# Performance work log

Measured on AMD Instinct MI355X. Metric: run time of the kernel, lower is better.

Reference implementation:

```python
import jax, jax.numpy as jnp
import numpy as np

EPS = 1e-5


def _bn(x, g, b):
    # BatchNorm1d in training mode: batch mean, biased variance, eps=1e-5
    m = jnp.mean(x, axis=0)
    v = jnp.var(x, axis=0)
    return (x - m) * jax.lax.rsqrt(v + EPS) * g + b


def setup_inputs() -> dict:
    key = jax.random.key(0)
    ks = jax.random.split(key, 16)
    B, N, F, H = 4096, 128, 4, 32
    w = lambda k, o, i: jax.random.normal(k, (o, i), jnp.float32) * 0.3
    d = {
        'u': jax.random.normal(ks[0], (B, N, F), jnp.float32),
        'mask': jnp.ones((B * N, 1), jnp.int32),
        # MLPphi params
        'p_bn1_g': jnp.ones((F,), jnp.float32), 'p_bn1_b': jnp.zeros((F,), jnp.float32), 'p_w1': w(ks[1], H, F),
        'p_bn2_g': jnp.ones((H,), jnp.float32), 'p_bn2_b': jnp.zeros((H,), jnp.float32), 'p_w2': w(ks[2], H, H),
        'p_bn3_g': jnp.ones((H,), jnp.float32), 'p_bn3_b': jnp.zeros((H,), jnp.float32), 'p_w3': w(ks[3], H, H),
        # MLPomega params
        'o_bn1_g': jnp.ones((F,), jnp.float32), 'o_bn1_b': jnp.zeros((F,), jnp.float32), 'o_w1': w(ks[4], H, F),
        'o_bn2_g': jnp.ones((H,), jnp.float32), 'o_bn2_b': jnp.zeros((H,), jnp.float32), 'o_w2': w(ks[5], H, H),
        'o_bn3_g': jnp.ones((H,), jnp.float32), 'o_bn3_b': jnp.zeros((H,), jnp.float32), 'o_w3': w(ks[6], H, H),
        # MLPtheta params
        't_bn1_g': jnp.ones((H,), jnp.float32), 't_bn1_b': jnp.zeros((H,), jnp.float32), 't_w1': w(ks[7], H, H),
        't_bn2_g': jnp.ones((H,), jnp.float32), 't_bn2_b': jnp.zeros((H,), jnp.float32), 't_w2': w(ks[8], H, H),
        't_bn3_g': jnp.ones((H,), jnp.float32), 't_bn3_b': jnp.zeros((H,), jnp.float32), 't_w3': w(ks[9], H, H),
        't_bn4_g': jnp.ones((H,), jnp.float32), 't_bn4_b': jnp.zeros((H,), jnp.float32),
        't_w4': w(ks[10], 1, H), 't_b4': jnp.zeros((1,), jnp.float32),
    }
    return d


def _forward(u, mask,
             p_bn1_g, p_bn1_b, p_w1, p_bn2_g, p_bn2_b, p_w2, p_bn3_g, p_bn3_b, p_w3,
             o_bn1_g, o_bn1_b, o_w1, o_bn2_g, o_bn2_b, o_w2, o_bn3_g, o_bn3_b, o_w3,
             t_bn1_g, t_bn1_b, t_w1, t_bn2_g, t_bn2_b, t_w2, t_bn3_g, t_bn3_b, t_w3,
             t_bn4_g, t_bn4_b, t_w4, t_b4):
    B, N, F = u.shape
    H = p_w1.shape[0]
    u_flat = u.reshape(-1, F)  # (B*N, F)

    # MLPphi: three BN+Linear(no bias)+Tanh blocks with residual adds (dropout=identity in eval)
    o1 = jnp.tanh(_bn(u_flat, p_bn1_g, p_bn1_b) @ p_w1.T)
    o2 = jnp.tanh(_bn(o1, p_bn2_g, p_bn2_b) @ p_w2.T)
    o3 = jnp.tanh(_bn(o1 + o2, p_bn3_g, p_bn3_b) @ p_w3.T)
    x_main = (o1 + o2 + o3).reshape(B, N, H)

    # MLPomega: BN+Linear+Tanh x2, BN+Linear, softmax over hidden dim (dim=1 of flat), then masked_fill
    a = jnp.tanh(_bn(u_flat, o_bn1_g, o_bn1_b) @ o_w1.T)
    a = jnp.tanh(_bn(a, o_bn2_g, o_bn2_b) @ o_w2.T)
    a = _bn(a, o_bn3_g, o_bn3_b) @ o_w3.T
    a = jax.nn.softmax(a, axis=1)
    a = jnp.where(mask == 0, -jnp.inf, a)
    x_attn = a.reshape(B, N, H)

    # attention pooling over neighbors
    x = jnp.sum(x_main * x_attn, axis=1)  # (B, H)

    x = jnp.tanh(_bn(x, t_bn1_g, t_bn1_b) @ t_w1.T)
    x = jnp.tanh(_bn(x, t_bn2_g, t_bn2_b) @ t_w2.T)
    x = jnp.tanh(_bn(x, t_bn3_g, t_bn3_b) @ t_w3.T)
    x = _bn(x, t_bn4_g, t_bn4_b) @ t_w4.T + t_b4
    return x


def reference(u, mask,
              p_bn1_g, p_bn1_b, p_w1, p_bn2_g, p_bn2_b, p_w2, p_bn3_g, p_bn3_b, p_w3,
              o_bn1_g, o_bn1_b, o_w1, o_bn2_g, o_bn2_b, o_w2, o_bn3_g, o_bn3_b, o_w3,
              t_bn1_g, t_bn1_b, t_w1, t_bn2_g, t_bn2_b, t_w2, t_bn3_g, t_bn3_b, t_w3,
              t_bn4_g, t_bn4_b, t_w4, t_b4):
    return _forward(u, mask,
                    p_bn1_g, p_bn1_b, p_w1, p_bn2_g, p_bn2_b, p_w2, p_bn3_g, p_bn3_b, p_w3,
                    o_bn1_g, o_bn1_b, o_w1, o_bn2_g, o_bn2_b, o_w2, o_bn3_g, o_bn3_b, o_w3,
                    t_bn1_g, t_bn1_b, t_w1, t_bn2_g, t_bn2_b, t_w2, t_bn3_g, t_bn3_b, t_w3,
                    t_bn4_g, t_bn4_b, t_w4, t_b4)
```

## Files before the change

### kernel.cpp

```cpp
#include <hip/hip_runtime.h>

typedef unsigned int u32;
typedef unsigned short u16;
typedef __attribute__((ext_vector_type(8))) _Float16 half8;
typedef __attribute__((ext_vector_type(4))) float f32x4;

#define ROWS  524288
#define BROWS 4096
#define EPS   1e-5f

#define S_U   0
#define S_O1  8
#define S_A1  72
#define S_O12 136
#define S_A2  200
#define S_X   264
#define S_X1  328
#define S_X2  392
#define S_X3  456
#define SHARD 1024
#define NSH   64

#define XSTR 40

__device__ __forceinline__ float bl(u32 u){ return __uint_as_float(u << 16); }
__device__ __forceinline__ float bh(u32 u){ return __uint_as_float(u & 0xFFFF0000u); }
__device__ __forceinline__ float b2f(u16 h){ return __uint_as_float(((u32)h) << 16); }
__device__ __forceinline__ u16 f2b(float f){
  u32 u = __float_as_uint(f);
  return (u16)((u + 0x7FFFu + ((u >> 16) & 1u)) >> 16);
}
__device__ __forceinline__ u16 f2h(float f){ _Float16 h = (_Float16)f; return __builtin_bit_cast(u16, h); }
__device__ __forceinline__ float h2f(u16 x){ return (float)__builtin_bit_cast(_Float16, x); }
__device__ __forceinline__ u32 pack2h(float a, float b){
  auto v = __builtin_amdgcn_cvt_pkrtz(a, b);
  return __builtin_bit_cast(u32, v);
}
__device__ __forceinline__ float lo16(u32 w){ return h2f((u16)(w & 0xFFFF)); }
__device__ __forceinline__ float hi16(u32 w){ return h2f((u16)(w >> 16)); }
__device__ __forceinline__ void unpk4(uint2 v, float* d){
  d[0]=lo16(v.x); d[1]=hi16(v.x); d[2]=lo16(v.y); d[3]=hi16(v.y);
}

__device__ __forceinline__ float tanh_fast(float x){
  float e = __expf(2.0f * x);
  return 1.0f - 2.0f * __builtin_amdgcn_rcpf(e + 1.0f);
}

template<bool F32>
__device__ __forceinline__ float rdp(const void* p, int i){
  if (F32) return ((const float*)p)[i];
  return b2f(((const u16*)p)[i]);
}
template<bool F32>
__device__ __forceinline__ void load_u4(const void* u, int r, float* f){
  if (F32){
    float4 v = ((const float4*)u)[r];
    f[0]=v.x; f[1]=v.y; f[2]=v.z; f[3]=v.w;
  } else {
    uint2 v = ((const uint2*)u)[r];
    f[0]=bl(v.x); f[1]=bh(v.x); f[2]=bl(v.y); f[3]=bh(v.y);
  }
}

__device__ __forceinline__ void g2lrow(const u16* __restrict__ g, int r, u16* X, int tid){
  const uint4* src = (const uint4*)&g[(size_t)r*32];
  uint4* dst = (uint4*)&X[tid*XSTR];
#pragma unroll
  for (int c=0;c<4;++c) dst[c] = src[c];
}
__device__ __forceinline__ void l2grow(const u16* X, int tid, u16* __restrict__ g, int r){
  const uint4* src = (const uint4*)&X[tid*XSTR];
  uint4* dst = (uint4*)&g[(size_t)r*32];
#pragma unroll
  for (int c=0;c<4;++c) dst[c] = src[c];
}

__global__ void k_detect(const u16* __restrict__ u, int* __restrict__ flag){
  int t = threadIdx.x;
  int bad = 0;
  for (int i = t*4; i < t*4+4; ++i){
    int e = (u[i] >> 7) & 0xFF;
    bad += (e >= 0x90) ? 1 : 0;
  }
#pragma unroll
  for (int off = 32; off >= 1; off >>= 1) bad += __shfl_down(bad, off);
  if (t == 0) *flag = (bad >= 4) ? 1 : 0;
}

template<bool F32>
__device__ __forceinline__ void stats_u_body(const void* __restrict__ u, float* __restrict__ S){
  int tid = blockIdx.x*blockDim.x + threadIdx.x;
  int nt  = gridDim.x*blockDim.x;
  float s[4]={0,0,0,0}, q[4]={0,0,0,0};
  for (int r = tid; r < ROWS; r += nt){
    float f[4]; load_u4<F32>(u, r, f);
#pragma unroll
    for (int k=0;k<4;++k){ s[k]+=f[k]; q[k]+=f[k]*f[k]; }
  }
#pragma unroll
  for (int off=32; off>=1; off>>=1){
#pragma unroll
    for (int k=0;k<4;++k){ s[k]+=__shfl_down(s[k],off); q[k]+=__shfl_down(q[k],off); }
  }
  if ((threadIdx.x & 63) == 0){
    float* Sh = S + (blockIdx.x & (NSH-1))*SHARD;
#pragma unroll
    for (int k=0;k<4;++k){ atomicAdd(&Sh[S_U+k], s[k]); atomicAdd(&Sh[S_U+4+k], q[k]); }
  }
}
__global__ __launch_bounds__(256) void k_stats_u(const void* __restrict__ u, float* __restrict__ S,
                                                 const int* __restrict__ flag){
  if (*flag) stats_u_body<true>(u,S); else stats_u_body<false>(u,S);
}

__device__ __forceinline__ void prep_u(const float* __restrict__ S, float* mr, int tid){
  if (tid < 4){
    float s=0.f, q=0.f;
    for (int sh=0; sh<NSH; ++sh){
      s += S[sh*SHARD + S_U + tid];
      q += S[sh*SHARD + S_U + 4 + tid];
    }
    float m = s*(1.0f/ROWS);
    float var = q*(1.0f/ROWS) - m*m;
    mr[tid]   = m;
    mr[4+tid] = rsqrtf(var + EPS);
  }
  __syncthreads();
}
template<bool F32>
__device__ __forceinline__ void bn_u_l(const float* mr, const void* g, const void* b,
                                       const float* f, float* xn){
#pragma unroll
  for (int k=0;k<4;++k)
    xn[k] = (f[k]-mr[k])*(rdp<F32>(g,k)*mr[4+k]) + rdp<F32>(b,k);
}

template<bool F32>
__device__ __forceinline__ void chain1_to_lds(const float* xn, const void* W1, u16* Xrow){
  u32 buf[16];
#pragma unroll
  for (int jp=0; jp<16; ++jp){
    int j0 = 2*jp, j1 = 2*jp+1;
    float a0 = tanh_fast(xn[0]*rdp<F32>(W1,j0*4+0) + xn[1]*rdp<F32>(W1,j0*4+1)
                       + xn[2]*rdp<F32>(W1,j0*4+2) + xn[3]*rdp<F32>(W1,j0*4+3));
    float a1 = tanh_fast(xn[0]*rdp<F32>(W1,j1*4+0) + xn[1]*rdp<F32>(W1,j1*4+1)
                       + xn[2]*rdp<F32>(W1,j1*4+2) + xn[3]*rdp<F32>(W1,j1*4+3));
    buf[jp] = pack2h(a0, a1);
  }
#pragma unroll
  for (int c=0;c<4;++c){
    uint4 v; v.x = buf[c*4]; v.y = buf[c*4+1]; v.z = buf[c*4+2]; v.w = buf[c*4+3];
    *(uint4*)&Xrow[c*8] = v;
  }
}

template<bool F32>
__device__ __forceinline__ void fold2(const float* __restrict__ S, int offA, int offB,
    const void* gA, const void* bA, const void* WA,
    const void* gB, const void* bB, const void* WB,
    u16* Wt, float* Cb, float* scr )
{
  int tid = threadIdx.x;
  if (tid < 64){
    int L = tid>>5, k = tid&31;
    const void* g = L? gB:gA; const void* b = L? bB:bA;
    int off = L? offB:offA;
    float s=0.f, q=0.f;
    for (int sh=0; sh<NSH; ++sh){
      s += S[sh*SHARD + off + k];
      q += S[sh*SHARD + off + 32 + k];
    }
    float m    = s*(1.0f/ROWS);
    float var  = q*(1.0f/ROWS) - m*m;
    float rstd = rsqrtf(var+EPS);
    float sc = rdp<F32>(g,k)*rstd;
    scr[tid]    = sc;
    scr[64+tid] = rdp<F32>(b,k) - m*sc;
  }
  __syncthreads();
  if (tid < 64){
    int L = tid>>5, j = tid&31;
    const void* W = L? WB:WA;
    float c = 0.f;
#pragma unroll
    for (int k=0;k<32;++k){
      float Wv = rdp<F32>(W, j*32+k);
      Wt[(L*32+j)*XSTR + k] = f2h(Wv * scr[(L<<5)|k]);
      c += Wv * scr[64 + ((L<<5)|k)];
    }
    Cb[L*32+j] = c;
  }
  __syncthreads();
}

template<bool F32>
__device__ __forceinline__ void fold4(const float* __restrict__ S,
    int off0,int off1,int off2,int off3,
    const void* g0,const void* b0,const void* W0,
    const void* g1,const void* b1,const void* W1,
    const void* g2,const void* b2,const void* W2,
    const void* g3,const void* b3,const void* W3,
    u16* Wt, float* Cb, float* scr )
{
  int tid = threadIdx.x;
  __shared__ float scr2[256];
  if (tid < 128){
    int L = tid>>5, k = tid&31;
    const void* g = (L==0)?g0:(L==1)?g1:(L==2)?g2:g3;
    const void* b = (L==0)?b0:(L==1)?b1:(L==2)?b2:b3;
    int off = (L==0)?off0:(L==1)?off1:(L==2)?off2:off3;
    float s=0.f, q=0.f;
    for (int sh=0; sh<NSH; ++sh){
      s += S[sh*SHARD + off + k];
      q += S[sh*SHARD + off + 32 + k];
    }
    float m    = s*(1.0f/ROWS);
    float var  = q*(1.0f/ROWS) - m*m;
    float rstd = rsqrtf(var+EPS);
    float sc = rdp<F32>(g,k)*rstd;
    scr[tid]  = sc;
    scr2[tid] = rdp<F32>(b,k) - m*sc;
  }
  __syncthreads();
  if (tid < 128){
    int L = tid>>5, j = tid&31;
    const void* W = (L==0)?W0:(L==1)?W1:(L==2)?W2:W3;
    float c = 0.f;
#pragma unroll
    for (int k=0;k<32;++k){
      float Wv = rdp<F32>(W, j*32+k);
      Wt[(L*32+j)*XSTR + k] = f2h(Wv * scr[(L<<5)|k]);
      c += Wv * scr2[(L<<5)|k];
    }
    Cb[L*32+j] = c;
  }
  __syncthreads();
}

#define KIND_TANH          0
#define KIND_TANHRES       2
#define KIND_TANHRES_ATREG 3
template<int KIND>
__device__ __forceinline__ void mfma_layer(u16* X, const u16* Wt, const float* Cb,
                                           int L, int wv, int lane, const u32* at_pk)
{
  int ln15 = lane & 15, quad = lane >> 4;
  half8 w0 = *(const half8*)&Wt[(L*32 + ln15     )*XSTR + quad*8];
  half8 w1 = *(const half8*)&Wt[(L*32 + ln15 + 16)*XSTR + quad*8];
  float bias0[4], bias1[4];
#pragma unroll
  for (int reg=0;reg<4;++reg){
    bias0[reg] = Cb[L*32 +      quad*4 + reg];
    bias1[reg] = Cb[L*32 + 16 + quad*4 + reg];
  }
  int rowbase = wv*64;
#pragma unroll
  for (int Mt=0; Mt<4; ++Mt){
    int s = rowbase + Mt*16 + ln15;
    half8 bfr = *(const half8*)&X[s*XSTR + quad*8];
    f32x4 c0 = {0.f,0.f,0.f,0.f}, c1 = {0.f,0.f,0.f,0.f};
    c0 = __builtin_amdgcn_mfma_f32_16x16x32_f16(w0, bfr, c0, 0,0,0);
    c1 = __builtin_amdgcn_mfma_f32_16x16x32_f16(w1, bfr, c1, 0,0,0);
    float o0[4], o1v[4];
    if (KIND == KIND_TANHRES || KIND == KIND_TANHRES_ATREG){
      unpk4(*(const uint2*)&X[s*XSTR +      quad*4], o0);
      unpk4(*(const uint2*)&X[s*XSTR + 16 + quad*4], o1v);
    }
    float a0v[4], a1v[4];
    if (KIND == KIND_TANHRES_ATREG){
      a0v[0]=lo16(at_pk[Mt*4+0]); a0v[1]=hi16(at_pk[Mt*4+0]);
      a0v[2]=lo16(at_pk[Mt*4+1]); a0v[3]=hi16(at_pk[Mt*4+1]);
      a1v[0]=lo16(at_pk[Mt*4+2]); a1v[1]=hi16(at_pk[Mt*4+2]);
      a1v[2]=lo16(at_pk[Mt*4+3]); a1v[3]=hi16(at_pk[Mt*4+3]);
    }
    float v0[4], v1[4];
#pragma unroll
    for (int reg=0;reg<4;++reg){
      float a = c0[reg] + bias0[reg];
      float b = c1[reg] + bias1[reg];
      if (KIND == KIND_TANH){ a = tanh_fast(a); b = tanh_fast(b); }
      else if (KIND == KIND_TANHRES){ a = o0[reg] + tanh_fast(a); b = o1v[reg] + tanh_fast(b); }
      else if (KIND == KIND_TANHRES_ATREG){
        a = (o0[reg] + tanh_fast(a)) * a0v[reg];
        b = (o1v[reg] + tanh_fast(b)) * a1v[reg];
      }
      v0[reg] = a; v1[reg] = b;
    }
    uint2 w0o, w1o;
    w0o.x = pack2h(v0[0], v0[1]); w0o.y = pack2h(v0[2], v0[3]);
    w1o.x = pack2h(v1[0], v1[1]); w1o.y = pack2h(v1[2], v1[3]);
    *(uint2*)&X[s*XSTR +      quad*4] = w0o;
    *(uint2*)&X[s*XSTR + 16 + quad*4] = w1o;
  }
}

__device__ __forceinline__ void mfma_logits_softmax(const u16* X, const u16* Wt, const float* Cb,
    int L, int wv, int lane, const int* __restrict__ mask, int maskbase, u32* at_pk)
{
  int ln15 = lane & 15, quad = lane >> 4;
  half8 w0 = *(const half8*)&Wt[(L*32 + ln15     )*XSTR + quad*8];
  half8 w1 = *(const half8*)&Wt[(L*32 + ln15 + 16)*XSTR + quad*8];
  float bias0[4], bias1[4];
#pragma unroll
  for (int reg=0;reg<4;++reg){
    bias0[reg] = Cb[L*32 +      quad*4 + reg];
    bias1[reg] = Cb[L*32 + 16 + quad*4 + reg];
  }
  int rowbase = wv*64;
#pragma unroll
  for (int Mt=0; Mt<4; ++Mt){
    int s = rowbase + Mt*16 + ln15;
    half8 bfr = *(const half8*)&X[s*XSTR + quad*8];
    f32x4 c0 = {0.f,0.f,0.f,0.f}, c1 = {0.f,0.f,0.f,0.f};
    c0 = __builtin_amdgcn_mfma_f32_16x16x32_f16(w0, bfr, c0, 0,0,0);
    c1 = __builtin_amdgcn_mfma_f32_16x16x32_f16(w1, bfr, c1, 0,0,0);
    float l0[4], l1[4];
#pragma unroll
    for (int reg=0;reg<4;++reg){ l0[reg] = c0[reg]+bias0[reg]; l1[reg] = c1[reg]+bias1[reg]; }
    float mx = l0[0];
#pragma unroll
    for (int reg=1;reg<4;++reg) mx = fmaxf(mx, l0[reg]);
#pragma unroll
    for (int reg=0;reg<4;++reg) mx = fmaxf(mx, l1[reg]);
    mx = fmaxf(mx, __shfl_xor(mx, 16));
    mx = fmaxf(mx, __shfl_xor(mx, 32));
    float sum = 0.f;
#pragma unroll
    for (int reg=0;reg<4;++reg){ l0[reg] = __expf(l0[reg]-mx); sum += l0[reg]; }
#pragma unroll
    for (int reg=0;reg<4;++reg){ l1[reg] = __expf(l1[reg]-mx); sum += l1[reg]; }
    sum += __shfl_xor(sum, 16);
    sum += __shfl_xor(sum, 32);
    float inv = __builtin_amdgcn_rcpf(sum);
    bool mz = (mask[maskbase + Mt*16 + ln15] == 0);
#pragma unroll
    for (int reg=0;reg<4;++reg){
      l0[reg] *= inv; l1[reg] *= inv;
      if (mz){ l0[reg] = -__builtin_inff(); l1[reg] = -__builtin_inff(); }
    }
    at_pk[Mt*4+0] = pack2h(l0[0], l0[1]);
    at_pk[Mt*4+1] = pack2h(l0[2], l0[3]);
    at_pk[Mt*4+2] = pack2h(l1[0], l1[1]);
    at_pk[Mt*4+3] = pack2h(l1[2], l1[3]);
  }
}

__device__ __forceinline__ void reduce_f16(const u16* X, float* lds2,
                                           float* __restrict__ S, int offS, int shard)
{
  int tid = threadIdx.x;
  __syncthreads();
  {
    int j = tid & 31, seg = tid >> 5;
    float s=0.f, q=0.f;
    for (int q2=0;q2<32;++q2){
      float v = h2f(X[(seg*32+q2)*XSTR + j]);
      s += v; q = fmaf(v,v,q);
    }
    lds2[seg*32+j] = s;
    lds2[256 + seg*32+j] = q;
  }
  __syncthreads();
  if (tid < 64){
    int j = tid & 31; bool isq = tid >= 32;
    const float* src = lds2 + (isq?256:0);
    float tot=0.f;
#pragma unroll
    for (int sg=0;sg<8;++sg) tot += src[sg*32+j];
    atomicAdd(&S[shard*SHARD + offS + (isq?32:0) + j], tot);
  }
  __syncthreads();
}

__device__ __forceinline__ void reduce_f32(const float* Xs, float* lds2,
                                           float* __restrict__ S, int offS, int shard)
{
  int tid = threadIdx.x;
  __syncthreads();
  {
    int j = tid & 31, seg = tid >> 5;
    float s=0.f, q=0.f;
    for (int q2=0;q2<32;++q2){
      float v = Xs[(seg*32+q2)*33 + j];
      s += v; q = fmaf(v,v,q);
    }
    lds2[seg*32+j] = s;
    lds2[256 + seg*32+j] = q;
  }
  __syncthreads();
  if (tid < 64){
    int j = tid & 31; bool isq = tid >= 32;
    const float* src = lds2 + (isq?256:0);
    float tot=0.f;
#pragma unroll
    for (int sg=0;sg<8;++sg) tot += src[sg*32+j];
    atomicAdd(&S[shard*SHARD + offS + (isq?32:0) + j], tot);
  }
  __syncthreads();
}

template<bool F32, bool MAT>
__device__ __forceinline__ void pass1_body(const void* __restrict__ u,
    const void* pg1, const void* pb1, const void* pw1,
    const void* og1, const void* ob1, const void* ow1,
    float* __restrict__ S, u16* __restrict__ o1g, u16* __restrict__ a1g,
    float* Xs, float* lds2, float* mr)
{
  int tid = threadIdx.x;
  int r = blockIdx.x*256 + tid;
  int shard = blockIdx.x & (NSH-1);
  prep_u(S, mr, tid);
  float f[4]; load_u4<F32>(u,r,f);
  float xn[4];
  float* Xp = Xs + tid*33;

  bn_u_l<F32>(mr, pg1, pb1, f, xn);
  {
    u32 buf[16];
#pragma unroll
    for (int jp=0;jp<16;++jp){
      int j0=2*jp, j1=2*jp+1;
      float a0 = tanh_fast(xn[0]*rdp<F32>(pw1,j0*4+0) + xn[1]*rdp<F32>(pw1,j0*4+1)
                         + xn[2]*rdp<F32>(pw1,j0*4+2) + xn[3]*rdp<F32>(pw1,j0*4+3));
      float a1 = tanh_fast(xn[0]*rdp<F32>(pw1,j1*4+0) + xn[1]*rdp<F32>(pw1,j1*4+1)
                         + xn[2]*rdp<F32>(pw1,j1*4+2) + xn[3]*rdp<F32>(pw1,j1*4+3));
      Xp[j0]=a0; Xp[j1]=a1;
      if (MAT) buf[jp] = pack2h(a0,a1);
    }
    if (MAT){
      uint4* dst = (uint4*)&o1g[(size_t)r*32];
#pragma unroll
      for (int c=0;c<4;++c){ uint4 v; v.x=buf[c*4]; v.y=buf[c*4+1]; v.z=buf[c*4+2]; v.w=buf[c*4+3]; dst[c]=v; }
    }
  }
  reduce_f32(Xs, lds2, S, S_O1, shard);

  bn_u_l<F32>(mr, og1, ob1, f, xn);
  {
    u32 buf[16];
#pragma unroll
    for (int jp=0;jp<16;++jp){
      int j0=2*jp, j1=2*jp+1;
      float a0 = tanh_fast(xn[0]*rdp<F32>(ow1,j0*4+0) + xn[1]*rdp<F32>(ow1,j0*4+1)
                         + xn[2]*rdp<F32>(ow1,j0*4+2) + xn[3]*rdp<F32>(ow1,j0*4+3));
      float a1 = tanh_fast(xn[0]*rdp<F32>(ow1,j1*4+0) + xn[1]*rdp<F32>(ow1,j1*4+1)
                         + xn[2]*rdp<F32>(ow1,j1*4+2) + xn[3]*rdp<F32>(ow1,j1*4+3));
      Xp[j0]=a0; Xp[j1]=a1;
      if (MAT) buf[jp] = pack2h(a0,a1);
    }
    if (MAT){
      uint4* dst = (uint4*)&a1g[(size_t)r*32];
#pragma unroll
      for (int c=0;c<4;++c){ uint4 v; v.x=buf[c*4]; v.y=buf[c*4+1]; v.z=buf[c*4+2]; v.w=buf[c*4+3]; dst[c]=v; }
    }
  }
  reduce_f32(Xs, lds2, S, S_A1, shard);
}
template<bool MAT>
__global__ __launch_bounds__(256) void k_pass1(const void* __restrict__ u,
    const void* pg1, const void* pb1, const void* pw1,
    const void* og1, const void* ob1, const void* ow1,
    float* __restrict__ S, u16* o1g, u16* a1g, const int* __restrict__ flag){
  __shared__ float Xs[256*33];
  __shared__ float lds2[512];
  __shared__ float mr[8];
  if (*flag) pass1_body<true ,MAT>(u,pg1,pb1,pw1,og1,ob1,ow1,S,o1g,a1g,Xs,lds2,mr);
  else       pass1_body<false,MAT>(u,pg1,pb1,pw1,og1,ob1,ow1,S,o1g,a1g,Xs,lds2,mr);
}

template<bool F32, bool MAT>
__device__ __forceinline__ void pass2_body(const void* __restrict__ u,
    const void* pg1, const void* pb1, const void* pw1,
    const void* og1, const void* ob1, const void* ow1,
    const void* pg2, const void* pb2, const void* pw2,
    const void* og2, const void* ob2, const void* ow2,
    float* __restrict__ S,
    const u16* __restrict__ o1g, const u16* __restrict__ a1g,
    u16* __restrict__ o12g, u16* __restrict__ a2g,
    u16* X, u16* Wt, float* Cb, float* lds2, float* mr)
{
  int tid = threadIdx.x;
  int wv = tid >> 6, lane = tid & 63;
  int r = blockIdx.x*256 + tid;
  int shard = blockIdx.x & (NSH-1);
  if (!MAT) prep_u(S, mr, tid);
  fold2<F32>(S, S_O1, S_A1, pg2,pb2,pw2, og2,ob2,ow2, Wt, Cb, lds2);

  float f[4], xn[4];
  if (!MAT) load_u4<F32>(u,r,f);

  if (MAT) g2lrow(o1g, r, X, tid);
  else { bn_u_l<F32>(mr, pg1, pb1, f, xn); chain1_to_lds<F32>(xn, pw1, X + tid*XSTR); }
  mfma_layer<KIND_TANHRES>(X, Wt, Cb, 0, wv, lane, 0);
  reduce_f16(X, lds2, S, S_O12, shard);
  if (MAT) l2grow(X, tid, o12g, r);

  if (MAT) g2lrow(a1g, r, X, tid);
  else { bn_u_l<F32>(mr, og1, ob1, f, xn); chain1_to_lds<F32>(xn, ow1, X + tid*XSTR); }
  mfma_layer<KIND_TANH  >(X, Wt, Cb, 1, wv, lane, 0);
  reduce_f16(X, lds2, S, S_A2, shard);
  if (MAT) l2grow(X, tid, a2g, r);
}
template<bool MAT>
__global__ __launch_bounds__(256) void k_pass2(const void* __restrict__ u,
    const void* pg1, const void* pb1, const void* pw1,
    const void* og1, const void* ob1, const void* ow1,
    const void* pg2, const void* pb2, const void* pw2,
    const void* og2, const void* ob2, const void* ow2,
    float* __restrict__ S, const u16* o1g, const u16* a1g, u16* o12g, u16* a2g,
    const int* __restrict__ flag){
  __shared__ u16 X[256*XSTR];
  __shared__ u16 Wt[2*32*XSTR];
  __shared__ float Cb[64];
  __shared__ float lds2[512];
  __shared__ float mr[8];
  if (*flag) pass2_body<true ,MAT>(u,pg1,pb1,pw1,og1,ob1,ow1,pg2,pb2,pw2,og2,ob2,ow2,S,o1g,a1g,o12g,a2g,X,Wt,Cb,lds2,mr);
  else       pass2_body<false,MAT>(u,pg1,pb1,pw1,og1,ob1,ow1,pg2,pb2,pw2,og2,ob2,ow2,S,o1g,a1g,o12g,a2g,X,Wt,Cb,lds2,mr);
}

template<bool F32, bool MAT>
__device__ __forceinline__ void pass3_body(const void* __restrict__ u, const int* __restrict__ mask,
    const void* pg1, const void* pb1, const void* pw1,
    const void* og1, const void* ob1, const void* ow1,
    const void* pg2, const void* pb2, const void* pw2,
    const void* og2, const void* ob2, const void* ow2,
    const void* pg3, const void* pb3, const void* pw3,
    const void* og3, const void* ob3, const void* ow3,
    const u16* __restrict__ o12g, const u16* __restrict__ a2g,
    float* __restrict__ x, float* __restrict__ S,
    u16* X, u16* Wt, float* Cb, float* red2, float* mr)
{
  int tid = threadIdx.x;
  int wv = tid >> 6, lane = tid & 63;
  int r = blockIdx.x*256 + tid;
  if (!MAT) prep_u(S, mr, tid);
  if (MAT){
    fold2<F32>(S, S_A2, S_O12, og3,ob3,ow3, pg3,pb3,pw3, Wt, Cb, red2);
  } else {
    fold4<F32>(S, S_A1, S_A2, S_O1, S_O12,
               og2,ob2,ow2, og3,ob3,ow3, pg2,pb2,pw2, pg3,pb3,pw3,
               Wt, Cb, red2);
  }

  float f[4], xn[4];
  if (!MAT) load_u4<F32>(u,r,f);
  u32 at_pk[16];
  int maskbase = blockIdx.x*256 + wv*64;

  if (MAT) g2lrow(a2g, r, X, tid);
  else { bn_u_l<F32>(mr, og1, ob1, f, xn); chain1_to_lds<F32>(xn, ow1, X + tid*XSTR);
         mfma_layer<KIND_TANH>(X, Wt, Cb, 0, wv, lane, 0); }
  mfma_logits_softmax(X, Wt, Cb, MAT?0:1, wv, lane, mask, maskbase, at_pk);

  if (MAT) g2lrow(o12g, r, X, tid);
  else { bn_u_l<F32>(mr, pg1, pb1, f, xn); chain1_to_lds<F32>(xn, pw1, X + tid*XSTR);
         mfma_layer<KIND_TANHRES>(X, Wt, Cb, 2, wv, lane, 0); }
  mfma_layer<KIND_TANHRES_ATREG>(X, Wt, Cb, MAT?1:3, wv, lane, at_pk);

  __syncthreads();
  {
    int jj = tid & 31, cgrp = (tid >> 5) & 3, half = tid >> 7;
    float s2 = 0.f;
    for (int q2=0;q2<32;++q2) s2 += h2f(X[(half*128 + cgrp*32 + q2)*XSTR + jj]);
    red2[tid] = s2;
  }
  __syncthreads();
  if (tid < 64){
    int half = tid >> 5, j = tid & 31;
    float v = red2[half*128+j] + red2[half*128+32+j] + red2[half*128+64+j] + red2[half*128+96+j];
    x[(blockIdx.x*2 + half)*32 + j] = v;
    float* Sh = S + (blockIdx.x & (NSH-1))*SHARD;
    atomicAdd(&Sh[S_X+j], v);
    atomicAdd(&Sh[S_X+32+j], v*v);
  }
}
template<bool MAT>
__global__ __launch_bounds__(256) void k_pass3(const void* __restrict__ u, const int* __restrict__ mask,
    const void* pg1, const void* pb1, const void* pw1,
    const void* og1, const void* ob1, const void* ow1,
    const void* pg2, const void* pb2, const void* pw2,
    const void* og2, const void* ob2, const void* ow2,
    const void* pg3, const void* pb3, const void* pw3,
    const void* og3, const void* ob3, const void* ow3,
    const u16* o12g, const u16* a2g,
    float* __restrict__ x, float* __restrict__ S, const int* __restrict__ flag){
  __shared__ u16 X [256*XSTR];
  __shared__ u16 Wt[4*32*XSTR];
  __shared__ float Cb[128];
  __shared__ float red2[256];
  __shared__ float mr[8];
  if (*flag) pass3_body<true ,MAT>(u,mask,pg1,pb1,pw1,og1,ob1,ow1,pg2,pb2,pw2,og2,ob2,ow2,
                                   pg3,pb3,pw3,og3,ob3,ow3,o12g,a2g,x,S,X,Wt,Cb,red2,mr);
  else       pass3_body<false,MAT>(u,mask,pg1,pb1,pw1,og1,ob1,ow1,pg2,pb2,pw2,og2,ob2,ow2,
                                   pg3,pb3,pw3,og3,ob3,ow3,o12g,a2g,x,S,X,Wt,Cb,red2,mr);
}

template<bool F32>
__device__ __forceinline__ void theta_body(const float* __restrict__ X, float* __restrict__ S, int offin,
    const void* g, const void* bt, const void* W, float* __restrict__ Y, int offout,
    float* lds, float* lds2)
{
  int r = blockIdx.x*blockDim.x + threadIdx.x;
  int tid = threadIdx.x;
  int shard = blockIdx.x & (NSH-1);
  if (tid < 32){
    float s=0.f, q=0.f;
    for (int sh=0; sh<NSH; ++sh){
      s += S[sh*SHARD + offin + tid];
      q += S[sh*SHARD + offin + 32 + tid];
    }
    float m = s*(1.0f/BROWS);
    float var = q*(1.0f/BROWS) - m*m;
    lds2[tid]    = m;
    lds2[32+tid] = rsqrtf(var + EPS);
  }
  __syncthreads();
  float* Xp = lds + tid*33;
#pragma unroll
  for (int k=0;k<32;++k){
    Xp[k] = (X[(size_t)r*32+k] - lds2[k]) * (rdp<F32>(g,k)*lds2[32+k]) + rdp<F32>(bt,k);
  }
  float out[32];
#pragma unroll
  for (int j=0;j<32;++j){
    float acc = 0.f;
#pragma unroll
    for (int k=0;k<32;++k) acc = fmaf(rdp<F32>(W, j*32+k), Xp[k], acc);
    out[j] = tanh_fast(acc);
    Y[(size_t)r*32+j] = out[j];
  }
  __syncthreads();
#pragma unroll
  for (int j=0;j<32;++j) Xp[j] = out[j];
  reduce_f32(lds, lds2, S, offout, shard);
}
__global__ __launch_bounds__(256) void k_theta(const float* X, float* S, int offin,
    const void* g, const void* bt, const void* W, float* Y, int offout, const int* __restrict__ flag){
  __shared__ float lds[256*33];
  __shared__ float lds2[512];
  if (*flag) theta_body<true >(X,S,offin,g,bt,W,Y,offout,lds,lds2);
  else       theta_body<false>(X,S,offin,g,bt,W,Y,offout,lds,lds2);
}

template<bool F32>
__device__ __forceinline__ void theta4_body(const float* __restrict__ X, const float* __restrict__ S, int offin,
    const void* g, const void* bt, const void* w4, const void* b4, void* out, float* ms)
{
  int r = blockIdx.x*blockDim.x + threadIdx.x;
  int tid = threadIdx.x;
  if (tid < 32){
    float s=0.f, q=0.f;
    for (int sh=0; sh<NSH; ++sh){
      s += S[sh*SHARD + offin + tid];
      q += S[sh*SHARD + offin + 32 + tid];
    }
    float m = s*(1.0f/BROWS);
    float var = q*(1.0f/BROWS) - m*m;
    ms[tid]    = m;
    ms[32+tid] = rsqrtf(var + EPS);
  }
  __syncthreads();
  float acc = rdp<F32>(b4, 0);
#pragma unroll
  for (int k=0;k<32;++k){
    float xnv = (X[(size_t)r*32+k] - ms[k]) * (rdp<F32>(g,k)*ms[32+k]) + rdp<F32>(bt,k);
    acc = fmaf(rdp<F32>(w4,k), xnv, acc);
  }
  if (F32) ((float*)out)[r] = acc;
  else     ((u16*)out)[r]  = f2b(acc);
}
__global__ __launch_bounds__(256) void k_theta4(const float* X, const float* S, int offin,
    const void* g, const void* bt, const void* w4, const void* b4, void* out, const int* __restrict__ flag){
  __shared__ float ms[64];
  if (*flag) theta4_body<true >(X,S,offin,g,bt,w4,b4,out,ms);
  else       theta4_body<false>(X,S,offin,g,bt,w4,b4,out,ms);
}

extern "C" void kernel_launch(void* const* d_in, const int* in_sizes, int n_in,
                              void* d_out, int out_size, void* d_ws, size_t ws_size,
                              hipStream_t stream)
{
  const void* u    = d_in[0];
  const int*  mask = (const int*)d_in[1];
  const void *pg1=d_in[2],  *pb1=d_in[3],  *pw1=d_in[4];
  const void *pg2=d_in[5],  *pb2=d_in[6],  *pw2=d_in[7];
  const void *pg3=d_in[8],  *pb3=d_in[9],  *pw3=d_in[10];
  const void *og1=d_in[11], *ob1=d_in[12], *ow1=d_in[13];
  const void *og2=d_in[14], *ob2=d_in[15], *ow2=d_in[16];
  const void *og3=d_in[17], *ob3=d_in[18], *ow3=d_in[19];
  const void *tg1=d_in[20], *tb1=d_in[21], *tw1=d_in[22];
  const void *tg2=d_in[23], *tb2=d_in[24], *tw2=d_in[25];
  const void *tg3=d_in[26], *tb3=d_in[27], *tw3=d_in[28];
  const void *tg4=d_in[29], *tb4=d_in[30], *tw4=d_in[31], *tbb4=d_in[32];

  char* ws = (char*)d_ws;
  int*   flag = (int*)ws;
  float* S    = (float*)(ws + 4096);
  float* x    = (float*)(ws + 524288);
  float* x1 = x  + BROWS*32;
  float* x2 = x1 + BROWS*32;
  float* x3 = x2 + BROWS*32;

  const size_t MB = 1024*1024;
  u16* o1g  = (u16*)(ws + 8*MB);
  u16* a1g  = (u16*)(ws + 40*MB);
  u16* o12g = (u16*)(ws + 72*MB);
  u16* a2g  = (u16*)(ws + 104*MB);
  bool MAT = ws_size >= 137*MB;

  (void)hipMemsetAsync(ws, 0, 4096 + NSH*SHARD*4, stream);
  k_detect<<<1, 64, 0, stream>>>((const u16*)u, flag);
  k_stats_u<<<512, 256, 0, stream>>>(u, S, flag);
  if (MAT){
    k_pass1<true ><<<2048, 256, 0, stream>>>(u, pg1,pb1,pw1, og1,ob1,ow1, S, o1g, a1g, flag);
    k_pass2<true ><<<2048, 256, 0, stream>>>(u, pg1,pb1,pw1, og1,ob1,ow1,
                                             pg2,pb2,pw2, og2,ob2,ow2, S, o1g, a1g, o12g, a2g, flag);
    k_pass3<true ><<<2048, 256, 0, stream>>>(u, mask, pg1,pb1,pw1, og1,ob1,ow1,
                                             pg2,pb2,pw2, og2,ob2,ow2,
                                             pg3,pb3,pw3, og3,ob3,ow3, o12g, a2g, x, S, flag);
  } else {
    k_pass1<false><<<2048, 256, 0, stream>>>(u, pg1,pb1,pw1, og1,ob1,ow1, S, o1g, a1g, flag);
    k_pass2<false><<<2048, 256, 0, stream>>>(u, pg1,pb1,pw1, og1,ob1,ow1,
                                             pg2,pb2,pw2, og2,ob2,ow2, S, o1g, a1g, o12g, a2g, flag);
    k_pass3<false><<<2048, 256, 0, stream>>>(u, mask, pg1,pb1,pw1, og1,ob1,ow1,
                                             pg2,pb2,pw2, og2,ob2,ow2,
                                             pg3,pb3,pw3, og3,ob3,ow3, o12g, a2g, x, S, flag);
  }
  k_theta<<<16, 256, 0, stream>>>(x,  S, S_X,  tg1,tb1,tw1, x1, S_X1, flag);
  k_theta<<<16, 256, 0, stream>>>(x1, S, S_X1, tg2,tb2,tw2, x2, S_X2, flag);
  k_theta<<<16, 256, 0, stream>>>(x2, S, S_X2, tg3,tb3,tw3, x3, S_X3, flag);
  k_theta4<<<16, 256, 0, stream>>>(x3, S, S_X3, tg4,tb4,tw4,tbb4, d_out, flag);
}
```

Before: 323.6 us.

## Drop fp16 activation materialization and always recompute early layers from input

Removes the workspace path that stored first- and second-layer activations to global memory as fp16 rows and reloaded them in later passes. Every pass now reloads the small input rows and recomputes the earlier BN+linear+tanh layers in registers and shared memory. This removes about 256 MB of round-trip global traffic across the three passes, at the cost of extra MFMA and tanh work in passes 2 and 3. The stats kernel grid is also doubled from 512 to 1024 blocks.

Measured after the change: 339.1 us. 4.8% more time.

```diff
diff --git a/kernel.cpp b/kernel.cpp
--- a/kernel.cpp
+++ b/kernel.cpp
@@ -63,19 +63,6 @@
   }
 }
 
-__device__ __forceinline__ void g2lrow(const u16* __restrict__ g, int r, u16* X, int tid){
-  const uint4* src = (const uint4*)&g[(size_t)r*32];
-  uint4* dst = (uint4*)&X[tid*XSTR];
-#pragma unroll
-  for (int c=0;c<4;++c) dst[c] = src[c];
-}
-__device__ __forceinline__ void l2grow(const u16* X, int tid, u16* __restrict__ g, int r){
-  const uint4* src = (const uint4*)&X[tid*XSTR];
-  uint4* dst = (uint4*)&g[(size_t)r*32];
-#pragma unroll
-  for (int c=0;c<4;++c) dst[c] = src[c];
-}
-
 __global__ void k_detect(const u16* __restrict__ u, int* __restrict__ flag){
   int t = threadIdx.x;
   int bad = 0;
@@ -400,12 +387,11 @@
   __syncthreads();
 }
 
-template<bool F32, bool MAT>
+template<bool F32>
 __device__ __forceinline__ void pass1_body(const void* __restrict__ u,
     const void* pg1, const void* pb1, const void* pw1,
     const void* og1, const void* ob1, const void* ow1,
-    float* __restrict__ S, u16* __restrict__ o1g, u16* __restrict__ a1g,
-    float* Xs, float* lds2, float* mr)
+    float* __restrict__ S, float* Xs, float* lds2, float* mr)
 {
   int tid = threadIdx.x;
   int r = blockIdx.x*256 + tid;
@@ -416,110 +402,74 @@
   float* Xp = Xs + tid*33;
 
   bn_u_l<F32>(mr, pg1, pb1, f, xn);
-  {
-    u32 buf[16];
-#pragma unroll
-    for (int jp=0;jp<16;++jp){
-      int j0=2*jp, j1=2*jp+1;
-      float a0 = tanh_fast(xn[0]*rdp<F32>(pw1,j0*4+0) + xn[1]*rdp<F32>(pw1,j0*4+1)
-                         + xn[2]*rdp<F32>(pw1,j0*4+2) + xn[3]*rdp<F32>(pw1,j0*4+3));
-      float a1 = tanh_fast(xn[0]*rdp<F32>(pw1,j1*4+0) + xn[1]*rdp<F32>(pw1,j1*4+1)
-                         + xn[2]*rdp<F32>(pw1,j1*4+2) + xn[3]*rdp<F32>(pw1,j1*4+3));
-      Xp[j0]=a0; Xp[j1]=a1;
-      if (MAT) buf[jp] = pack2h(a0,a1);
-    }
-    if (MAT){
-      uint4* dst = (uint4*)&o1g[(size_t)r*32];
-#pragma unroll
-      for (int c=0;c<4;++c){ uint4 v; v.x=buf[c*4]; v.y=buf[c*4+1]; v.z=buf[c*4+2]; v.w=buf[c*4+3]; dst[c]=v; }
-    }
-  }
+#pragma unroll
+  for (int j=0;j<32;++j)
+    Xp[j] = tanh_fast(xn[0]*rdp<F32>(pw1,j*4+0) + xn[1]*rdp<F32>(pw1,j*4+1)
+                    + xn[2]*rdp<F32>(pw1,j*4+2) + xn[3]*rdp<F32>(pw1,j*4+3));
   reduce_f32(Xs, lds2, S, S_O1, shard);
 
   bn_u_l<F32>(mr, og1, ob1, f, xn);
-  {
-    u32 buf[16];
-#pragma unroll
-    for (int jp=0;jp<16;++jp){
-      int j0=2*jp, j1=2*jp+1;
-      float a0 = tanh_fast(xn[0]*rdp<F32>(ow1,j0*4+0) + xn[1]*rdp<F32>(ow1,j0*4+1)
-                         + xn[2]*rdp<F32>(ow1,j0*4+2) + xn[3]*rdp<F32>(ow1,j0*4+3));
-      float a1 = tanh_fast(xn[0]*rdp<F32>(ow1,j1*4+0) + xn[1]*rdp<F32>(ow1,j1*4+1)
-                         + xn[2]*rdp<F32>(ow1,j1*4+2) + xn[3]*rdp<F32>(ow1,j1*4+3));
-      Xp[j0]=a0; Xp[j1]=a1;
-      if (MAT) buf[jp] = pack2h(a0,a1);
-    }
-    if (MAT){
-      uint4* dst = (uint4*)&a1g[(size_t)r*32];
-#pragma unroll
-      for (int c=0;c<4;++c){ uint4 v; v.x=buf[c*4]; v.y=buf[c*4+1]; v.z=buf[c*4+2]; v.w=buf[c*4+3]; dst[c]=v; }
-    }
-  }
+#pragma unroll
+  for (int j=0;j<32;++j)
+    Xp[j] = tanh_fast(xn[0]*rdp<F32>(ow1,j*4+0) + xn[1]*rdp<F32>(ow1,j*4+1)
+                    + xn[2]*rdp<F32>(ow1,j*4+2) + xn[3]*rdp<F32>(ow1,j*4+3));
   reduce_f32(Xs, lds2, S, S_A1, shard);
 }
-template<bool MAT>
 __global__ __launch_bounds__(256) void k_pass1(const void* __restrict__ u,
     const void* pg1, const void* pb1, const void* pw1,
     const void* og1, const void* ob1, const void* ow1,
-    float* __restrict__ S, u16* o1g, u16* a1g, const int* __restrict__ flag){
+    float* __restrict__ S, const int* __restrict__ flag){
   __shared__ float Xs[256*33];
   __shared__ float lds2[512];
   __shared__ float mr[8];
-  if (*flag) pass1_body<true ,MAT>(u,pg1,pb1,pw1,og1,ob1,ow1,S,o1g,a1g,Xs,lds2,mr);
-  else       pass1_body<false,MAT>(u,pg1,pb1,pw1,og1,ob1,ow1,S,o1g,a1g,Xs,lds2,mr);
-}
-
-template<bool F32, bool MAT>
+  if (*flag) pass1_body<true >(u,pg1,pb1,pw1,og1,ob1,ow1,S,Xs,lds2,mr);
+  else       pass1_body<false>(u,pg1,pb1,pw1,og1,ob1,ow1,S,Xs,lds2,mr);
+}
+
+template<bool F32>
 __device__ __forceinline__ void pass2_body(const void* __restrict__ u,
     const void* pg1, const void* pb1, const void* pw1,
     const void* og1, const void* ob1, const void* ow1,
     const void* pg2, const void* pb2, const void* pw2,
     const void* og2, const void* ob2, const void* ow2,
-    float* __restrict__ S,
-    const u16* __restrict__ o1g, const u16* __restrict__ a1g,
-    u16* __restrict__ o12g, u16* __restrict__ a2g,
-    u16* X, u16* Wt, float* Cb, float* lds2, float* mr)
+    float* __restrict__ S, u16* X, u16* Wt, float* Cb, float* lds2, float* mr)
 {
   int tid = threadIdx.x;
   int wv = tid >> 6, lane = tid & 63;
   int r = blockIdx.x*256 + tid;
   int shard = blockIdx.x & (NSH-1);
-  if (!MAT) prep_u(S, mr, tid);
+  prep_u(S, mr, tid);
   fold2<F32>(S, S_O1, S_A1, pg2,pb2,pw2, og2,ob2,ow2, Wt, Cb, lds2);
 
   float f[4], xn[4];
-  if (!MAT) load_u4<F32>(u,r,f);
-
-  if (MAT) g2lrow(o1g, r, X, tid);
-  else { bn_u_l<F32>(mr, pg1, pb1, f, xn); chain1_to_lds<F32>(xn, pw1, X + tid*XSTR); }
+  load_u4<F32>(u,r,f);
+
+  bn_u_l<F32>(mr, pg1, pb1, f, xn);
+  chain1_to_lds<F32>(xn, pw1, X + tid*XSTR);
   mfma_layer<KIND_TANHRES>(X, Wt, Cb, 0, wv, lane, 0);
   reduce_f16(X, lds2, S, S_O12, shard);
-  if (MAT) l2grow(X, tid, o12g, r);
-
-  if (MAT) g2lrow(a1g, r, X, tid);
-  else { bn_u_l<F32>(mr, og1, ob1, f, xn); chain1_to_lds<F32>(xn, ow1, X + tid*XSTR); }
+
+  bn_u_l<F32>(mr, og1, ob1, f, xn);
+  chain1_to_lds<F32>(xn, ow1, X + tid*XSTR);
   mfma_layer<KIND_TANH  >(X, Wt, Cb, 1, wv, lane, 0);
   reduce_f16(X, lds2, S, S_A2, shard);
-  if (MAT) l2grow(X, tid, a2g, r);
-}
-template<bool MAT>
+}
 __global__ __launch_bounds__(256) void k_pass2(const void* __restrict__ u,
     const void* pg1, const void* pb1, const void* pw1,
     const void* og1, const void* ob1, const void* ow1,
     const void* pg2, const void* pb2, const void* pw2,
     const void* og2, const void* ob2, const void* ow2,
-    float* __restrict__ S, const u16* o1g, const u16* a1g, u16* o12g, u16* a2g,
-    const int* __restrict__ flag){
+    float* __restrict__ S, const int* __restrict__ flag){
   __shared__ u16 X[256*XSTR];
   __shared__ u16 Wt[2*32*XSTR];
   __shared__ float Cb[64];
   __shared__ float lds2[512];
   __shared__ float mr[8];
-  if (*flag) pass2_body<true ,MAT>(u,pg1,pb1,pw1,og1,ob1,ow1,pg2,pb2,pw2,og2,ob2,ow2,S,o1g,a1g,o12g,a2g,X,Wt,Cb,lds2,mr);
-  else       pass2_body<false,MAT>(u,pg1,pb1,pw1,og1,ob1,ow1,pg2,pb2,pw2,og2,ob2,ow2,S,o1g,a1g,o12g,a2g,X,Wt,Cb,lds2,mr);
-}
-
-template<bool F32, bool MAT>
+  if (*flag) pass2_body<true >(u,pg1,pb1,pw1,og1,ob1,ow1,pg2,pb2,pw2,og2,ob2,ow2,S,X,Wt,Cb,lds2,mr);
+  else       pass2_body<false>(u,pg1,pb1,pw1,og1,ob1,ow1,pg2,pb2,pw2,og2,ob2,ow2,S,X,Wt,Cb,lds2,mr);
+}
+
+template<bool F32>
 __device__ __forceinline__ void pass3_body(const void* __restrict__ u, const int* __restrict__ mask,
     const void* pg1, const void* pb1, const void* pw1,
     const void* og1, const void* ob1, const void* ow1,
@@ -527,36 +477,31 @@
     const void* og2, const void* ob2, const void* ow2,
     const void* pg3, const void* pb3, const void* pw3,
     const void* og3, const void* ob3, const void* ow3,
-    const u16* __restrict__ o12g, const u16* __restrict__ a2g,
     float* __restrict__ x, float* __restrict__ S,
     u16* X, u16* Wt, float* Cb, float* red2, float* mr)
 {
   int tid = threadIdx.x;
   int wv = tid >> 6, lane = tid & 63;
   int r = blockIdx.x*256 + tid;
-  if (!MAT) prep_u(S, mr, tid);
-  if (MAT){
-    fold2<F32>(S, S_A2, S_O12, og3,ob3,ow3, pg3,pb3,pw3, Wt, Cb, red2);
-  } else {
-    fold4<F32>(S, S_A1, S_A2, S_O1, S_O12,
-               og2,ob2,ow2, og3,ob3,ow3, pg2,pb2,pw2, pg3,pb3,pw3,
-               Wt, Cb, red2);
-  }
+  prep_u(S, mr, tid);
+  fold4<F32>(S, S_A1, S_A2, S_O1, S_O12,
+             og2,ob2,ow2, og3,ob3,ow3, pg2,pb2,pw2, pg3,pb3,pw3,
+             Wt, Cb, red2);
 
   float f[4], xn[4];
-  if (!MAT) load_u4<F32>(u,r,f);
+  load_u4<F32>(u,r,f);
   u32 at_pk[16];
   int maskbase = blockIdx.x*256 + wv*64;
 
-  if (MAT) g2lrow(a2g, r, X, tid);
-  else { bn_u_l<F32>(mr, og1, ob1, f, xn); chain1_to_lds<F32>(xn, ow1, X + tid*XSTR);
-         mfma_layer<KIND_TANH>(X, Wt, Cb, 0, wv, lane, 0); }
-  mfma_logits_softmax(X, Wt, Cb, MAT?0:1, wv, lane, mask, maskbase, at_pk);
-
-  if (MAT) g2lrow(o12g, r, X, tid);
-  else { bn_u_l<F32>(mr, pg1, pb1, f, xn); chain1_to_lds<F32>(xn, pw1, X + tid*XSTR);
-         mfma_layer<KIND_TANHRES>(X, Wt, Cb, 2, wv, lane, 0); }
-  mfma_layer<KIND_TANHRES_ATREG>(X, Wt, Cb, MAT?1:3, wv, lane, at_pk);
+  bn_u_l<F32>(mr, og1, ob1, f, xn);
+  chain1_to_lds<F32>(xn, ow1, X + tid*XSTR);
+  mfma_layer<KIND_TANH>(X, Wt, Cb, 0, wv, lane, 0);
+  mfma_logits_softmax(X, Wt, Cb, 1, wv, lane, mask, maskbase, at_pk);
+
+  bn_u_l<F32>(mr, pg1, pb1, f, xn);
+  chain1_to_lds<F32>(xn, pw1, X + tid*XSTR);
+  mfma_layer<KIND_TANHRES   >(X, Wt, Cb, 2, wv, lane, 0);
+  mfma_layer<KIND_TANHRES_ATREG>(X, Wt, Cb, 3, wv, lane, at_pk);
 
   __syncthreads();
   {
@@ -575,7 +520,6 @@
     atomicAdd(&Sh[S_X+32+j], v*v);
   }
 }
-template<bool MAT>
 __global__ __launch_bounds__(256) void k_pass3(const void* __restrict__ u, const int* __restrict__ mask,
     const void* pg1, const void* pb1, const void* pw1,
     const void* og1, const void* ob1, const void* ow1,
@@ -583,17 +527,16 @@
     const void* og2, const void* ob2, const void* ow2,
     const void* pg3, const void* pb3, const void* pw3,
     const void* og3, const void* ob3, const void* ow3,
-    const u16* o12g, const u16* a2g,
     float* __restrict__ x, float* __restrict__ S, const int* __restrict__ flag){
   __shared__ u16 X [256*XSTR];
   __shared__ u16 Wt[4*32*XSTR];
   __shared__ float Cb[128];
   __shared__ float red2[256];
   __shared__ float mr[8];
-  if (*flag) pass3_body<true ,MAT>(u,mask,pg1,pb1,pw1,og1,ob1,ow1,pg2,pb2,pw2,og2,ob2,ow2,
-                                   pg3,pb3,pw3,og3,ob3,ow3,o12g,a2g,x,S,X,Wt,Cb,red2,mr);
-  else       pass3_body<false,MAT>(u,mask,pg1,pb1,pw1,og1,ob1,ow1,pg2,pb2,pw2,og2,ob2,ow2,
-                                   pg3,pb3,pw3,og3,ob3,ow3,o12g,a2g,x,S,X,Wt,Cb,red2,mr);
+  if (*flag) pass3_body<true >(u,mask,pg1,pb1,pw1,og1,ob1,ow1,pg2,pb2,pw2,og2,ob2,ow2,
+                               pg3,pb3,pw3,og3,ob3,ow3,x,S,X,Wt,Cb,red2,mr);
+  else       pass3_body<false>(u,mask,pg1,pb1,pw1,og1,ob1,ow1,pg2,pb2,pw2,og2,ob2,ow2,
+                               pg3,pb3,pw3,og3,ob3,ow3,x,S,X,Wt,Cb,red2,mr);
 }
 
 template<bool F32>
@@ -702,31 +645,15 @@
   float* x2 = x1 + BROWS*32;
   float* x3 = x2 + BROWS*32;
 
-  const size_t MB = 1024*1024;
-  u16* o1g  = (u16*)(ws + 8*MB);
-  u16* a1g  = (u16*)(ws + 40*MB);
-  u16* o12g = (u16*)(ws + 72*MB);
-  u16* a2g  = (u16*)(ws + 104*MB);
-  bool MAT = ws_size >= 137*MB;
-
   (void)hipMemsetAsync(ws, 0, 4096 + NSH*SHARD*4, stream);
   k_detect<<<1, 64, 0, stream>>>((const u16*)u, flag);
-  k_stats_u<<<512, 256, 0, stream>>>(u, S, flag);
-  if (MAT){
-    k_pass1<true ><<<2048, 256, 0, stream>>>(u, pg1,pb1,pw1, og1,ob1,ow1, S, o1g, a1g, flag);
-    k_pass2<true ><<<2048, 256, 0, stream>>>(u, pg1,pb1,pw1, og1,ob1,ow1,
-                                             pg2,pb2,pw2, og2,ob2,ow2, S, o1g, a1g, o12g, a2g, flag);
-    k_pass3<true ><<<2048, 256, 0, stream>>>(u, mask, pg1,pb1,pw1, og1,ob1,ow1,
-                                             pg2,pb2,pw2, og2,ob2,ow2,
-                                             pg3,pb3,pw3, og3,ob3,ow3, o12g, a2g, x, S, flag);
-  } else {
-    k_pass1<false><<<2048, 256, 0, stream>>>(u, pg1,pb1,pw1, og1,ob1,ow1, S, o1g, a1g, flag);
-    k_pass2<false><<<2048, 256, 0, stream>>>(u, pg1,pb1,pw1, og1,ob1,ow1,
-                                             pg2,pb2,pw2, og2,ob2,ow2, S, o1g, a1g, o12g, a2g, flag);
-    k_pass3<false><<<2048, 256, 0, stream>>>(u, mask, pg1,pb1,pw1, og1,ob1,ow1,
-                                             pg2,pb2,pw2, og2,ob2,ow2,
-                                             pg3,pb3,pw3, og3,ob3,ow3, o12g, a2g, x, S, flag);
-  }
+  k_stats_u<<<1024, 256, 0, stream>>>(u, S, flag);
+  k_pass1<<<2048, 256, 0, stream>>>(u, pg1,pb1,pw1, og1,ob1,ow1, S, flag);
+  k_pass2<<<2048, 256, 0, stream>>>(u, pg1,pb1,pw1, og1,ob1,ow1,
+                                    pg2,pb2,pw2, og2,ob2,ow2, S, flag);
+  k_pass3<<<2048, 256, 0, stream>>>(u, mask, pg1,pb1,pw1, og1,ob1,ow1,
+                                    pg2,pb2,pw2, og2,ob2,ow2,
+                                    pg3,pb3,pw3, og3,ob3,ow3, x, S, flag);
   k_theta<<<16, 256, 0, stream>>>(x,  S, S_X,  tg1,tb1,tw1, x1, S_X1, flag);
   k_theta<<<16, 256, 0, stream>>>(x1, S, S_X1, tg2,tb2,tw2, x2, S_X2, flag);
   k_theta<<<16, 256, 0, stream>>>(x2, S, S_X2, tg3,tb3,tw3, x3, S_X3, flag);
```
